# Optimization experiments

Measured on AMD Instinct MI355X. Metric: run time of the kernel, lower is better.

## Reference

```python
import jax, jax.numpy as jnp
import numpy as np

N_NODES = 30000
N_EDGES = 480000
N_GRAPHS = 500
D_IN = 78


def gcn_conv(x, W, b, src, dst, n_nodes):
    """PyG GCNConv: add self-loops, sym-normalize, linear then aggregate, bias after."""
    xw = x @ W  # [N, d_out]
    deg = jnp.zeros((n_nodes,), x.dtype).at[dst].add(1.0) + 1.0  # +1 self-loop
    dinv = jax.lax.rsqrt(deg)
    norm = dinv[src] * dinv[dst]  # [E]
    msg = xw[src] * norm[:, None]  # [E, d_out] edge gather
    out = jnp.zeros_like(xw).at[dst].add(msg)  # scatter-add to dst
    out = out + xw * (dinv * dinv)[:, None]  # self-loop contribution
    return out + b


def setup_inputs() -> dict:
    key = jax.random.key(0)
    ks = jax.random.split(key, 16)
    x = jax.random.normal(ks[0], (N_NODES, D_IN), dtype=jnp.float32)
    edge_index = jax.random.randint(ks[1], (2, N_EDGES), 0, N_NODES, dtype=jnp.int32)
    batch = jnp.sort(jax.random.randint(ks[2], (N_NODES,), 0, N_GRAPHS, dtype=jnp.int32))

    def lin(k, fi, fo):
        s = 1.0 / np.sqrt(fi)
        k1, k2 = jax.random.split(k)
        W = jax.random.uniform(k1, (fi, fo), jnp.float32, -s, s)
        b = jax.random.uniform(k2, (fo,), jnp.float32, -s, s)
        return W, b

    W1, b1 = lin(ks[3], D_IN, D_IN)
    W2, b2 = lin(ks[4], D_IN, D_IN * 2)
    W3, b3 = lin(ks[5], D_IN * 2, D_IN * 4)
    Wf1, bf1 = lin(ks[6], D_IN * 4, 1024)
    Wf2, bf2 = lin(ks[7], 1024, 128)
    return {"x": x, "edge_index": edge_index, "batch": batch,
            "W1": W1, "b1": b1, "W2": W2, "b2": b2, "W3": W3, "b3": b3,
            "Wf1": Wf1, "bf1": bf1, "Wf2": Wf2, "bf2": bf2}


def reference(x, edge_index, batch, W1, b1, W2, b2, W3, b3, Wf1, bf1, Wf2, bf2):
    src, dst = edge_index[0], edge_index[1]
    n = x.shape[0]
    h = jax.nn.relu(gcn_conv(x, W1, b1, src, dst, n))
    h = jax.nn.relu(gcn_conv(h, W2, b2, src, dst, n))
    h = jax.nn.relu(gcn_conv(h, W3, b3, src, dst, n))
    # global max pool over graphs
    pooled = jax.ops.segment_max(h, batch, num_segments=N_GRAPHS)  # [G, 312]
    pooled = jnp.where(jnp.isfinite(pooled), pooled, 0.0)  # guard empty segments
    out = jax.nn.relu(pooled @ Wf1 + bf1)
    out = out @ Wf2 + bf2  # dropout is identity in eval mode
    return out
```

## Files before the change

### kernel.cpp

```cpp
#include <hip/hip_runtime.h>

#define NODES  30000
#define EDGES  480000
#define GRAPHS 500
#define MPAD   30016
#define NB     118

typedef __bf16 bf16x8 __attribute__((ext_vector_type(8)));
typedef float  f32x4  __attribute__((ext_vector_type(4)));
typedef _Float16 half8v __attribute__((ext_vector_type(8)));
typedef unsigned short ushort8v __attribute__((ext_vector_type(8)));

__device__ __forceinline__ float4 f4max(float4 a, float4 b) {
    a.x = fmaxf(a.x, b.x); a.y = fmaxf(a.y, b.y);
    a.z = fmaxf(a.z, b.z); a.w = fmaxf(a.w, b.w); return a;
}

__device__ __forceinline__ void split_f32(float a, unsigned short& hi, unsigned short& lo) {
    unsigned int u = __float_as_uint(a);
    unsigned int rh = (u + 0x7fffu + ((u >> 16) & 1u)) & 0xffff0000u;
    hi = (unsigned short)(rh >> 16);
    float l = a - __uint_as_float(rh);
    unsigned int ul = __float_as_uint(l);
    lo = (unsigned short)((ul + 0x7fffu + ((ul >> 16) & 1u)) >> 16);
}

__device__ __forceinline__ void gload_lds16(const void* g, void* l) {
    __builtin_amdgcn_global_load_lds(
        (__attribute__((address_space(1))) void*)g,
        (__attribute__((address_space(3))) void*)l, 16, 0, 0);
}

__global__ __launch_bounds__(256) void prep_kernel(
    const float* __restrict__ W1, const float* __restrict__ W2, const float* __restrict__ W3,
    unsigned short* __restrict__ h1, unsigned short* __restrict__ l1,
    unsigned short* __restrict__ h2, unsigned short* __restrict__ l2,
    unsigned short* __restrict__ h3, unsigned short* __restrict__ l3,
    const int* __restrict__ dst, int* __restrict__ cnt)
{
    int b = blockIdx.x, t = threadIdx.x;
    if (b < 640) {
        const float* W; unsigned short *oh, *ol; int n, K, N, Kp;
        if (b < 128)      { W = W1; oh = h1; ol = l1; n = b;       K = 78;  N = 78;  Kp = 96;  }
        else if (b < 320) { W = W2; oh = h2; ol = l2; n = b - 128; K = 78;  N = 156; Kp = 96;  }
        else              { W = W3; oh = h3; ol = l3; n = b - 320; K = 156; N = 312; Kp = 160; }
        if (t < Kp) {
            float v = (n < N && t < K) ? W[(size_t)t * N + n] : 0.0f;
            unsigned short h, l;
            split_f32(v, h, l);
            oh[(size_t)n * Kp + t] = h;
            ol[(size_t)n * Kp + t] = l;
        }
    } else {
        int i = (b - 640) * 256 + t;
        if (i < EDGES) atomicAdd(&cnt[dst[i]], 1);
    }
}

__global__ __launch_bounds__(256) void scan_bsum_kernel(const int* __restrict__ cnt,
                                                        int* __restrict__ bsum, int n) {
    __shared__ int buf[256];
    int t = threadIdx.x;
    int i = blockIdx.x * 256 + t;
    buf[t] = (i < n) ? cnt[i] : 0;
    __syncthreads();
    for (int ofs = 128; ofs > 0; ofs >>= 1) {
        if (t < ofs) buf[t] += buf[t + ofs];
        __syncthreads();
    }
    if (t == 0) bsum[blockIdx.x] = buf[0];
}

__global__ __launch_bounds__(128) void scan_top_kernel(const int* __restrict__ bsum,
                                                       int* __restrict__ boff) {
    __shared__ int buf[128];
    int t = threadIdx.x;
    int own = (t < NB) ? bsum[t] : 0;
    buf[t] = own;
    __syncthreads();
    for (int ofs = 1; ofs < 128; ofs <<= 1) {
        int v = (t >= ofs) ? buf[t - ofs] : 0;
        __syncthreads();
        buf[t] += v;
        __syncthreads();
    }
    if (t < NB) boff[t] = buf[t] - own;
}

__global__ __launch_bounds__(256) void scan_apply_kernel(const int* __restrict__ cnt,
                                                         const int* __restrict__ boff,
                                                         int* __restrict__ rowstart,
                                                         int* __restrict__ cursor,
                                                         float* __restrict__ dinv, int n) {
    __shared__ int buf[256];
    int t = threadIdx.x;
    int i = blockIdx.x * 256 + t;
    int own = (i < n) ? cnt[i] : 0;
    buf[t] = own;
    __syncthreads();
    for (int ofs = 1; ofs < 256; ofs <<= 1) {
        int v = (t >= ofs) ? buf[t - ofs] : 0;
        __syncthreads();
        buf[t] += v;
        __syncthreads();
    }
    if (i < n) {
        rowstart[i] = boff[blockIdx.x] + buf[t] - own;
        cursor[i] = 0;
        dinv[i] = rsqrtf((float)own + 1.0f);
    }
}

__global__ __launch_bounds__(256) void fill_prescale_kernel(
    const int* __restrict__ src, const int* __restrict__ dst,
    const int* __restrict__ rowstart, int* __restrict__ cursor, int* __restrict__ csr_src,
    const float* __restrict__ X, const float* __restrict__ dinv,
    unsigned short* __restrict__ Xs16)
{
    int b = blockIdx.x, t = threadIdx.x;
    if (b < 1875) {
        int i = b * 256 + t;
        if (i < EDGES) {
            int d = dst[i];
            int pos = atomicAdd(&cursor[d], 1);
            csr_src[rowstart[d] + pos] = src[i];
        }
    } else {
        int i = (b - 1875) * 256 + t;
        if (i < NODES * 80) {
            int node = i / 80;
            int c = i - node * 80;
            float v = (c < 78) ? X[node * 78 + c] * dinv[node] : 0.0f;
            _Float16 hv = (_Float16)v;
            Xs16[i] = __builtin_bit_cast(unsigned short, hv);
        }
    }
}

template <int DVH, int KQH>
__global__ __launch_bounds__(256) void agg_half(
    const unsigned short* __restrict__ Xh, const int* __restrict__ rowstart,
    const int* __restrict__ cnt, const int* __restrict__ csr_src,
    const float* __restrict__ dinv,
    unsigned short* __restrict__ ohi, unsigned short* __restrict__ olo)
{
    constexpr int EPI = 64 / DVH;
    constexpr int Kp = KQH * 8;
    static_assert(EPI > 1, "EPI must exceed 1");
    int node = blockIdx.x * 4 + (threadIdx.x >> 6);
    int lane = threadIdx.x & 63;
    int sub = lane / DVH;
    int c = lane - sub * DVH;
    const half8v* X8 = (const half8v*)Xh;

    float acc0[8] = {}, acc1[8] = {};
    int s = rowstart[node];
    int e = s + cnt[node];

    if (sub < EPI) {
        if (sub == 0) {
            half8v v = X8[(size_t)node * DVH + c];
            #pragma unroll
            for (int i = 0; i < 8; i++) acc0[i] += (float)v[i];
        }
        int j = s;
        for (; j + 4 * EPI <= e; j += 4 * EPI) {
            int i0 = csr_src[j + sub],           i1 = csr_src[j + EPI + sub];
            int i2 = csr_src[j + 2 * EPI + sub], i3 = csr_src[j + 3 * EPI + sub];
            half8v x0 = X8[(size_t)i0 * DVH + c], x1 = X8[(size_t)i1 * DVH + c];
            half8v x2 = X8[(size_t)i2 * DVH + c], x3 = X8[(size_t)i3 * DVH + c];
            #pragma unroll
            for (int i = 0; i < 8; i++) {
                acc0[i] += (float)x0[i] + (float)x2[i];
                acc1[i] += (float)x1[i] + (float)x3[i];
            }
        }
        for (; j + 2 * EPI <= e; j += 2 * EPI) {
            int i0 = csr_src[j + sub], i1 = csr_src[j + EPI + sub];
            half8v x0 = X8[(size_t)i0 * DVH + c], x1 = X8[(size_t)i1 * DVH + c];
            #pragma unroll
            for (int i = 0; i < 8; i++) { acc0[i] += (float)x0[i]; acc1[i] += (float)x1[i]; }
        }
        for (; j < e; j += EPI) {
            int jj = j + sub;
            if (jj < e) {
                half8v x = X8[(size_t)csr_src[jj] * DVH + c];
                #pragma unroll
                for (int i = 0; i < 8; i++) acc0[i] += (float)x[i];
            }
        }
    }
    float acc[8];
    #pragma unroll
    for (int i = 0; i < 8; i++) acc[i] = acc0[i] + acc1[i];

    {
        float tmp[EPI - 1][8];
        #pragma unroll
        for (int sft = 1; sft < EPI; sft++)
            #pragma unroll
            for (int i = 0; i < 8; i++)
                tmp[sft - 1][i] = __shfl(acc[i], lane + sft * DVH);
        #pragma unroll
        for (int sft = 1; sft < EPI; sft++)
            #pragma unroll
            for (int i = 0; i < 8; i++)
                acc[i] += tmp[sft - 1][i];
    }

    if (lane < KQH) {
        float di = (lane < DVH) ? dinv[node] : 0.0f;
        ushort8v h8, l8;
        #pragma unroll
        for (int i = 0; i < 8; i++) {
            unsigned short hh, ll;
            split_f32(acc[i] * di, hh, ll);
            h8[i] = hh; l8[i] = ll;
        }
        size_t off = (size_t)node * Kp + (size_t)lane * 8;
        *(ushort8v*)&ohi[off] = h8;
        *(ushort8v*)&olo[off] = l8;
    }
}

template <int NCK, int OUT16>
__global__ __launch_bounds__(256) void mfma_gemm_v2(
    const unsigned short* __restrict__ Ahi, const unsigned short* __restrict__ Alo,
    const unsigned short* __restrict__ Bhi, const unsigned short* __restrict__ Blo,
    const float* __restrict__ bias, const float* __restrict__ scale,
    float* __restrict__ C, int M, int N, int Cstride, int nN, int do_relu)
{
    constexpr int Kp = NCK * 32;
    constexpr int CELLS = NCK * 256;
    extern __shared__ unsigned short smem[];
    unsigned short* sA = smem;
    unsigned short* sB = smem + 2 * CELLS * 8;

    int t = threadIdx.x;
    int wv = t >> 6, ln = t & 63;
    int q = ln >> 4, l16 = ln & 15;
    int wm = wv & 1, wn = wv >> 1;
    int m0 = blockIdx.x * 64;

    #pragma unroll
    for (int i = 0; i < 2 * NCK; i++) {
        int c = i * 256 + t;
        int plane = c / CELLS;
        int r = c - plane * CELLS;
        int ck = r >> 8, qq = (r >> 6) & 3, row = r & 63;
        const unsigned short* src = (plane ? Alo : Ahi) + (size_t)(m0 + row) * Kp + ck * 32 + qq * 8;
        gload_lds16(src, &sA[(size_t)c * 8]);
    }

    for (int nt = 0; nt < nN; nt++) {
        int n0 = nt * 64;
        if (nt > 0) __syncthreads();
        #pragma unroll
        for (int i = 0; i < 2 * NCK; i++) {
            int c = i * 256 + t;
            int plane = c / CELLS;
            int r = c - plane * CELLS;
            int ck = r >> 8, qq = (r >> 6) & 3, row = r & 63;
            const unsigned short* src = (plane ? Blo : Bhi) + (size_t)(n0 + row) * Kp + ck * 32 + qq * 8;
            gload_lds16(src, &sB[(size_t)c * 8]);
        }
        __syncthreads();

        f32x4 acc[2][2] = {};
        #pragma unroll
        for (int ck = 0; ck < NCK; ck++) {
            bf16x8 ah[2], al[2], bh[2], bl[2];
            #pragma unroll
            for (int i = 0; i < 2; i++) {
                int ra = wm * 32 + i * 16 + l16;
                int rb = wn * 32 + i * 16 + l16;
                ah[i] = *(const bf16x8*)&sA[(size_t)(((0 * NCK + ck) * 4 + q) * 64 + ra) * 8];
                al[i] = *(const bf16x8*)&sA[(size_t)(((1 * NCK + ck) * 4 + q) * 64 + ra) * 8];
                bh[i] = *(const bf16x8*)&sB[(size_t)(((0 * NCK + ck) * 4 + q) * 64 + rb) * 8];
                bl[i] = *(const bf16x8*)&sB[(size_t)(((1 * NCK + ck) * 4 + q) * 64 + rb) * 8];
            }
            #pragma unroll
            for (int i = 0; i < 2; i++)
                #pragma unroll
                for (int j = 0; j < 2; j++) {
                    acc[i][j] = __builtin_amdgcn_mfma_f32_16x16x32_bf16(ah[i], bh[j], acc[i][j], 0, 0, 0);
                    acc[i][j] = __builtin_amdgcn_mfma_f32_16x16x32_bf16(ah[i], bl[j], acc[i][j], 0, 0, 0);
                    acc[i][j] = __builtin_amdgcn_mfma_f32_16x16x32_bf16(al[i], bh[j], acc[i][j], 0, 0, 0);
                }
        }

        #pragma unroll
        for (int i = 0; i < 2; i++) {
            int rbase = m0 + wm * 32 + i * 16 + q * 4;
            #pragma unroll
            for (int j = 0; j < 2; j++) {
                int col = n0 + wn * 32 + j * 16 + l16;
                if (col >= Cstride) continue;
                float bv = (col < N) ? bias[col] : 0.0f;
                #pragma unroll
                for (int r = 0; r < 4; r++) {
                    int row = rbase + r;
                    if (row < M) {
                        float v = 0.0f;
                        if (col < N) {
                            v = acc[i][j][r] + bv;
                            if (do_relu) v = fmaxf(v, 0.0f);
                            if (scale) v *= scale[row];
                        }
                        if constexpr (OUT16) {
                            _Float16 hv = (_Float16)v;
                            ((unsigned short*)C)[(size_t)row * Cstride + col] =
                                __builtin_bit_cast(unsigned short, hv);
                        } else {
                            C[(size_t)row * Cstride + col] = v;
                        }
                    }
                }
            }
        }
    }
}

__device__ inline int lower_bound_dev(const int* a, int n, int v) {
    int lo = 0, hi = n;
    while (lo < hi) { int mid = (lo + hi) >> 1; if (a[mid] < v) lo = mid + 1; else hi = mid; }
    return lo;
}

__global__ __launch_bounds__(256) void pool_kernel(const float* __restrict__ H,
                                                   const int* __restrict__ batch,
                                                   float* __restrict__ pooled, int n, int G) {
    __shared__ float4 red[3][78];
    int g = blockIdx.x;
    int t = threadIdx.x;
    int s = lower_bound_dev(batch, n, g);
    int e = lower_bound_dev(batch, n, g + 1);
    int rg = t / 78, c = t - rg * 78;
    const float4* H4 = (const float4*)H;
    if (rg < 3) {
        float4 m = {0.f, 0.f, 0.f, 0.f};
        for (int i = s + rg; i < e; i += 3)
            m = f4max(m, H4[(size_t)i * 78 + c]);
        red[rg][c] = m;
    }
    __syncthreads();
    if (t < 78) {
        float4 m = f4max(f4max(red[0][t], red[1][t]), red[2][t]);
        ((float4*)pooled)[(size_t)g * 78 + t] = m;
    }
}

__global__ __launch_bounds__(256) void fc1_kernel(const float* __restrict__ pooled,
                                                  const float* __restrict__ Wf1,
                                                  const float* __restrict__ bf1,
                                                  float* __restrict__ f1buf) {
    __shared__ float pl[4][312];
    int cb = blockIdx.x, gb = blockIdx.y;
    int t = threadIdx.x;
    for (int i = t; i < 4 * 312; i += 256) {
        int g = i / 312, k = i - g * 312;
        pl[g][k] = pooled[(size_t)(gb * 4 + g) * 312 + k];
    }
    __syncthreads();
    int col = cb * 256 + t;
    float a0 = 0.f, a1 = 0.f, a2 = 0.f, a3 = 0.f;
    #pragma unroll 4
    for (int k = 0; k < 312; k++) {
        float w = Wf1[(size_t)k * 1024 + col];
        a0 += pl[0][k] * w; a1 += pl[1][k] * w; a2 += pl[2][k] * w; a3 += pl[3][k] * w;
    }
    float b = bf1[col];
    int g0 = gb * 4;
    f1buf[(size_t)g0 * 1024 + col]       = fmaxf(a0 + b, 0.f);
    f1buf[(size_t)(g0 + 1) * 1024 + col] = fmaxf(a1 + b, 0.f);
    f1buf[(size_t)(g0 + 2) * 1024 + col] = fmaxf(a2 + b, 0.f);
    f1buf[(size_t)(g0 + 3) * 1024 + col] = fmaxf(a3 + b, 0.f);
}

__global__ __launch_bounds__(256) void fc2_part_kernel(const float* __restrict__ f1buf,
                                                       const float* __restrict__ Wf2,
                                                       float* __restrict__ partial) {
    __shared__ float f1s[4][128];
    __shared__ float red[256][4];
    int kt = blockIdx.x;
    int gb = blockIdx.y;
    int t = threadIdx.x;
    int col = t & 127, ks = t >> 7;
    for (int i = t; i < 512; i += 256) {
        int g = i >> 7, k = i & 127;
        f1s[g][k] = f1buf[(size_t)(gb * 4 + g) * 1024 + kt * 128 + k];
    }
    __syncthreads();
    float a0 = 0.f, a1 = 0.f, a2 = 0.f, a3 = 0.f;
    const float* w2 = Wf2 + (size_t)(kt * 128 + ks * 64) * 128 + col;
    #pragma unroll 4
    for (int k = 0; k < 64; k++) {
        float w = w2[(size_t)k * 128];
        int kk = ks * 64 + k;
        a0 += f1s[0][kk] * w; a1 += f1s[1][kk] * w; a2 += f1s[2][kk] * w; a3 += f1s[3][kk] * w;
    }
    red[t][0] = a0; red[t][1] = a1; red[t][2] = a2; red[t][3] = a3;
    __syncthreads();
    if (t < 128) {
        #pragma unroll
        for (int g = 0; g < 4; g++)
            partial[((size_t)kt * GRAPHS + gb * 4 + g) * 128 + col] = red[t][g] + red[t + 128][g];
    }
}

__global__ void fc2_reduce_kernel(const float* __restrict__ partial, const float* __restrict__ bf2,
                                  float* __restrict__ out, int total) {
    int i = blockIdx.x * blockDim.x + threadIdx.x;
    if (i < total) {
        float s = bf2[i & 127];
        #pragma unroll
        for (int kt = 0; kt < 8; kt++) s += partial[(size_t)kt * total + i];
        out[i] = s;
    }
}

extern "C" void kernel_launch(void* const* d_in, const int* in_sizes, int n_in,
                              void* d_out, int out_size, void* d_ws, size_t ws_size,
                              hipStream_t stream) {
    const float* x    = (const float*)d_in[0];
    const int*   ei   = (const int*)d_in[1];
    const int*   batch= (const int*)d_in[2];
    const float* W1 = (const float*)d_in[3];  const float* b1  = (const float*)d_in[4];
    const float* W2 = (const float*)d_in[5];  const float* b2  = (const float*)d_in[6];
    const float* W3 = (const float*)d_in[7];  const float* b3  = (const float*)d_in[8];
    const float* Wf1= (const float*)d_in[9];  const float* bf1 = (const float*)d_in[10];
    const float* Wf2= (const float*)d_in[11]; const float* bf2 = (const float*)d_in[12];
    float* out = (float*)d_out;

    const int* srcp = ei;
    const int* dstp = ei + EDGES;

    char* p = (char*)d_ws;
    size_t o = 0;
    auto takeB = [&](size_t bytes) { char* q = p + o; o += (bytes + 255) & ~(size_t)255; return q; };
    int*   cnt      = (int*)takeB(NODES * 4);
    int*   cursor   = (int*)takeB(NODES * 4);
    int*   rowstart = (int*)takeB(NODES * 4);
    int*   bsum     = (int*)takeB(NB * 4);
    int*   boff     = (int*)takeB(NB * 4);
    float* dinv     = (float*)takeB(NODES * 4);
    int*   csr_src  = (int*)takeB(EDGES * 4);
    unsigned short* aggH = (unsigned short*)takeB((size_t)MPAD * 160 * 2);
    unsigned short* aggL = (unsigned short*)takeB((size_t)MPAD * 160 * 2);
    unsigned short* xs16 = (unsigned short*)takeB((size_t)MPAD * 80 * 2);
    float* hbuf    = (float*)takeB((size_t)NODES * 312 * 4);
    unsigned short* h16_1 = (unsigned short*)takeB((size_t)MPAD * 80 * 2);
    unsigned short* h16_2 = (unsigned short*)takeB((size_t)MPAD * 160 * 2);
    float* pooled  = (float*)takeB((size_t)GRAPHS * 312 * 4);
    float* f1buf   = (float*)takeB((size_t)GRAPHS * 1024 * 4);
    float* partial = (float*)takeB((size_t)8 * GRAPHS * 128 * 4);
    unsigned short* Wt1h = (unsigned short*)takeB(128 * 96 * 2);
    unsigned short* Wt1l = (unsigned short*)takeB(128 * 96 * 2);
    unsigned short* Wt2h = (unsigned short*)takeB(192 * 96 * 2);
    unsigned short* Wt2l = (unsigned short*)takeB(192 * 96 * 2);
    unsigned short* Wt3h = (unsigned short*)takeB(320 * 160 * 2);
    unsigned short* Wt3l = (unsigned short*)takeB(320 * 160 * 2);
    (void)ws_size;

    hipMemsetAsync(cnt, 0, NODES * sizeof(int), stream);

    prep_kernel<<<640 + 1875, 256, 0, stream>>>(W1, W2, W3, Wt1h, Wt1l, Wt2h, Wt2l,
                                                Wt3h, Wt3l, dstp, cnt);
    scan_bsum_kernel<<<NB, 256, 0, stream>>>(cnt, bsum, NODES);
    scan_top_kernel<<<1, 128, 0, stream>>>(bsum, boff);
    scan_apply_kernel<<<NB, 256, 0, stream>>>(cnt, boff, rowstart, cursor, dinv, NODES);
    fill_prescale_kernel<<<1875 + 9375, 256, 0, stream>>>(srcp, dstp, rowstart, cursor,
                                                          csr_src, x, dinv, xs16);

    const int NBLK = MPAD / 64;
    const int AGRID = NODES / 4;

    agg_half<10, 12><<<AGRID, 256, 0, stream>>>(xs16, rowstart, cnt, csr_src, dinv, aggH, aggL);
    mfma_gemm_v2<3, 1><<<NBLK, 256, 3 * 16384, stream>>>(aggH, aggL, Wt1h, Wt1l, b1, dinv,
                                                         (float*)h16_1, NODES, 78, 80, 2, 1);
    agg_half<10, 12><<<AGRID, 256, 0, stream>>>(h16_1, rowstart, cnt, csr_src, dinv, aggH, aggL);
    mfma_gemm_v2<3, 1><<<NBLK, 256, 3 * 16384, stream>>>(aggH, aggL, Wt2h, Wt2l, b2, dinv,
                                                         (float*)h16_2, NODES, 156, 160, 3, 1);
    agg_half<20, 20><<<AGRID, 256, 0, stream>>>(h16_2, rowstart, cnt, csr_src, dinv, aggH, aggL);
    mfma_gemm_v2<5, 0><<<NBLK, 256, 5 * 16384, stream>>>(aggH, aggL, Wt3h, Wt3l, b3, nullptr,
                                                         hbuf, NODES, 312, 312, 5, 1);

    pool_kernel<<<GRAPHS, 256, 0, stream>>>(hbuf, batch, pooled, NODES, GRAPHS);
    fc1_kernel<<<dim3(4, GRAPHS / 4), 256, 0, stream>>>(pooled, Wf1, bf1, f1buf);
    fc2_part_kernel<<<dim3(8, GRAPHS / 4), 256, 0, stream>>>(f1buf, Wf2, partial);
    fc2_reduce_kernel<<<(GRAPHS * 128 + 255) / 256, 256, 0, stream>>>(partial, bf2, out, GRAPHS * 128);
}
```

Before: 314.4 us.

## Store layer-3 output as fp16 for pooling and fuse fc2 partial/reduce

The third GCN GEMM now writes half-precision output instead of fp32, and the max-pool kernel reads half8 vectors and converts them to float. This halves the write and read traffic of the largest activation tensor, at the cost of fp16 rounding of the final node features. Separately, the fc2 split-K partial kernel and its reduce kernel are merged into one 512-thread kernel that reduces in shared memory and adds the bias, removing one launch and the partial buffer round trip.

```diff
diff --git a/kernel.cpp b/kernel.cpp
--- a/kernel.cpp
+++ b/kernel.cpp
@@ -10,11 +10,6 @@
 typedef float  f32x4  __attribute__((ext_vector_type(4)));
 typedef _Float16 half8v __attribute__((ext_vector_type(8)));
 typedef unsigned short ushort8v __attribute__((ext_vector_type(8)));
-
-__device__ __forceinline__ float4 f4max(float4 a, float4 b) {
-    a.x = fmaxf(a.x, b.x); a.y = fmaxf(a.y, b.y);
-    a.z = fmaxf(a.z, b.z); a.w = fmaxf(a.w, b.w); return a;
-}
 
 __device__ __forceinline__ void split_f32(float a, unsigned short& hi, unsigned short& lo) {
     unsigned int u = __float_as_uint(a);
@@ -327,26 +322,39 @@
     return lo;
 }
 
-__global__ __launch_bounds__(256) void pool_kernel(const float* __restrict__ H,
-                                                   const int* __restrict__ batch,
-                                                   float* __restrict__ pooled, int n, int G) {
-    __shared__ float4 red[3][78];
+__global__ __launch_bounds__(256) void pool_h16_kernel(const unsigned short* __restrict__ H,
+                                                       const int* __restrict__ batch,
+                                                       float* __restrict__ pooled, int n, int G) {
+    __shared__ float red[6][39][8];
     int g = blockIdx.x;
     int t = threadIdx.x;
     int s = lower_bound_dev(batch, n, g);
     int e = lower_bound_dev(batch, n, g + 1);
-    int rg = t / 78, c = t - rg * 78;
-    const float4* H4 = (const float4*)H;
-    if (rg < 3) {
-        float4 m = {0.f, 0.f, 0.f, 0.f};
-        for (int i = s + rg; i < e; i += 3)
-            m = f4max(m, H4[(size_t)i * 78 + c]);
-        red[rg][c] = m;
-    }
-    __syncthreads();
-    if (t < 78) {
-        float4 m = f4max(f4max(red[0][t], red[1][t]), red[2][t]);
-        ((float4*)pooled)[(size_t)g * 78 + t] = m;
+    int rg = t / 39, c = t - rg * 39;
+    const half8v* H8 = (const half8v*)H;
+    if (rg < 6) {
+        float m[8] = {0.f, 0.f, 0.f, 0.f, 0.f, 0.f, 0.f, 0.f};
+        for (int i = s + rg; i < e; i += 6) {
+            half8v v = H8[(size_t)i * 39 + c];
+            #pragma unroll
+            for (int j = 0; j < 8; j++) m[j] = fmaxf(m[j], (float)v[j]);
+        }
+        #pragma unroll
+        for (int j = 0; j < 8; j++) red[rg][c][j] = m[j];
+    }
+    __syncthreads();
+    if (t < 39) {
+        float m[8];
+        #pragma unroll
+        for (int j = 0; j < 8; j++) m[j] = red[0][t][j];
+        #pragma unroll
+        for (int r = 1; r < 6; r++)
+            #pragma unroll
+            for (int j = 0; j < 8; j++) m[j] = fmaxf(m[j], red[r][t][j]);
+        float4 a = {m[0], m[1], m[2], m[3]};
+        float4 b = {m[4], m[5], m[6], m[7]};
+        ((float4*)pooled)[(size_t)g * 78 + t * 2]     = a;
+        ((float4*)pooled)[(size_t)g * 78 + t * 2 + 1] = b;
     }
 }
 
@@ -377,45 +385,41 @@
     f1buf[(size_t)(g0 + 3) * 1024 + col] = fmaxf(a3 + b, 0.f);
 }
 
-__global__ __launch_bounds__(256) void fc2_part_kernel(const float* __restrict__ f1buf,
-                                                       const float* __restrict__ Wf2,
-                                                       float* __restrict__ partial) {
-    __shared__ float f1s[4][128];
-    __shared__ float red[256][4];
-    int kt = blockIdx.x;
-    int gb = blockIdx.y;
-    int t = threadIdx.x;
+__global__ __launch_bounds__(512) void fc2_kernel(
+    const float* __restrict__ f1buf, const float* __restrict__ Wf2,
+    const float* __restrict__ bf2, float* __restrict__ out)
+{
+    __shared__ float f1s[4][1024];
+    __shared__ float red[4][128][4];
+    int gb = blockIdx.x;
+    int t = threadIdx.x;
+    const float4* F4 = (const float4*)(f1buf + (size_t)gb * 4 * 1024);
+    #pragma unroll
+    for (int i = 0; i < 2; i++) {
+        int idx = i * 512 + t;
+        ((float4*)f1s)[idx] = F4[idx];
+    }
+    __syncthreads();
     int col = t & 127, ks = t >> 7;
-    for (int i = t; i < 512; i += 256) {
-        int g = i >> 7, k = i & 127;
-        f1s[g][k] = f1buf[(size_t)(gb * 4 + g) * 1024 + kt * 128 + k];
-    }
-    __syncthreads();
     float a0 = 0.f, a1 = 0.f, a2 = 0.f, a3 = 0.f;
-    const float* w2 = Wf2 + (size_t)(kt * 128 + ks * 64) * 128 + col;
+    const float* w2 = Wf2 + (size_t)(ks * 256) * 128 + col;
     #pragma unroll 4
-    for (int k = 0; k < 64; k++) {
+    for (int k = 0; k < 256; k++) {
         float w = w2[(size_t)k * 128];
-        int kk = ks * 64 + k;
-        a0 += f1s[0][kk] * w; a1 += f1s[1][kk] * w; a2 += f1s[2][kk] * w; a3 += f1s[3][kk] * w;
-    }
-    red[t][0] = a0; red[t][1] = a1; red[t][2] = a2; red[t][3] = a3;
+        int kk = ks * 256 + k;
+        a0 += f1s[0][kk] * w; a1 += f1s[1][kk] * w;
+        a2 += f1s[2][kk] * w; a3 += f1s[3][kk] * w;
+    }
+    red[ks][col][0] = a0; red[ks][col][1] = a1;
+    red[ks][col][2] = a2; red[ks][col][3] = a3;
     __syncthreads();
     if (t < 128) {
-        #pragma unroll
-        for (int g = 0; g < 4; g++)
-            partial[((size_t)kt * GRAPHS + gb * 4 + g) * 128 + col] = red[t][g] + red[t + 128][g];
-    }
-}
-
-__global__ void fc2_reduce_kernel(const float* __restrict__ partial, const float* __restrict__ bf2,
-                                  float* __restrict__ out, int total) {
-    int i = blockIdx.x * blockDim.x + threadIdx.x;
-    if (i < total) {
-        float s = bf2[i & 127];
-        #pragma unroll
-        for (int kt = 0; kt < 8; kt++) s += partial[(size_t)kt * total + i];
-        out[i] = s;
+        float b = bf2[t];
+        #pragma unroll
+        for (int g = 0; g < 4; g++) {
+            float s = b + red[0][t][g] + red[1][t][g] + red[2][t][g] + red[3][t][g];
+            out[(size_t)(gb * 4 + g) * 128 + t] = s;
+        }
     }
 }
 
@@ -448,12 +452,11 @@
     unsigned short* aggH = (unsigned short*)takeB((size_t)MPAD * 160 * 2);
     unsigned short* aggL = (unsigned short*)takeB((size_t)MPAD * 160 * 2);
     unsigned short* xs16 = (unsigned short*)takeB((size_t)MPAD * 80 * 2);
-    float* hbuf    = (float*)takeB((size_t)NODES * 312 * 4);
     unsigned short* h16_1 = (unsigned short*)takeB((size_t)MPAD * 80 * 2);
     unsigned short* h16_2 = (unsigned short*)takeB((size_t)MPAD * 160 * 2);
+    unsigned short* h16_3 = (unsigned short*)takeB((size_t)NODES * 312 * 2);
     float* pooled  = (float*)takeB((size_t)GRAPHS * 312 * 4);
     float* f1buf   = (float*)takeB((size_t)GRAPHS * 1024 * 4);
-    float* partial = (float*)takeB((size_t)8 * GRAPHS * 128 * 4);
     unsigned short* Wt1h = (unsigned short*)takeB(128 * 96 * 2);
     unsigned short* Wt1l = (unsigned short*)takeB(128 * 96 * 2);
     unsigned short* Wt2h = (unsigned short*)takeB(192 * 96 * 2);
@@ -482,11 +485,10 @@
     mfma_gemm_v2<3, 1><<<NBLK, 256, 3 * 16384, stream>>>(aggH, aggL, Wt2h, Wt2l, b2, dinv,
                                                          (float*)h16_2, NODES, 156, 160, 3, 1);
     agg_half<20, 20><<<AGRID, 256, 0, stream>>>(h16_2, rowstart, cnt, csr_src, dinv, aggH, aggL);
-    mfma_gemm_v2<5, 0><<<NBLK, 256, 5 * 16384, stream>>>(aggH, aggL, Wt3h, Wt3l, b3, nullptr,
-                                                         hbuf, NODES, 312, 312, 5, 1);
-
-    pool_kernel<<<GRAPHS, 256, 0, stream>>>(hbuf, batch, pooled, NODES, GRAPHS);
+    mfma_gemm_v2<5, 1><<<NBLK, 256, 5 * 16384, stream>>>(aggH, aggL, Wt3h, Wt3l, b3, nullptr,
+                                                         (float*)h16_3, NODES, 312, 312, 5, 1);
+
+    pool_h16_kernel<<<GRAPHS, 256, 0, stream>>>(h16_3, batch, pooled, NODES, GRAPHS);
     fc1_kernel<<<dim3(4, GRAPHS / 4), 256, 0, stream>>>(pooled, Wf1, bf1, f1buf);
-    fc2_part_kernel<<<dim3(8, GRAPHS / 4), 256, 0, stream>>>(f1buf, Wf2, partial);
-    fc2_reduce_kernel<<<(GRAPHS * 128 + 255) / 256, 256, 0, stream>>>(partial, bf2, out, GRAPHS * 128);
-}
+    fc2_kernel<<<GRAPHS / 4, 512, 0, stream>>>(f1buf, Wf2, bf2, out);
+}
```

Measured after the change: 319.4 us. No clear change (+1.6%).
